# Kernel optimization log

Measured on AMD Instinct MI355X. Metric: run time of the kernel, lower is better.

The kernel has to match this reference:

```python
import jax, jax.numpy as jnp
import numpy as np

B, N, D = 8, 65536, 3
K = 64                 # num_centers
NPOINT = 4096
M = NPOINT // K * 2    # max_neighbors = 128
S = NPOINT // K        # fps samples per group = 64
NITER = 10             # KMeans default Niter


def _sqdist(src, dst):
    # ||s||^2 + ||d||^2 - 2 s.d   (same math as (s-d)^2 sum, GEMM form)
    s2 = (src ** 2).sum(-1)[:, :, None]          # [B,N,1]
    d2 = (dst ** 2).sum(-1)[:, None, :]          # [B,1,K]
    return s2 + d2 - 2.0 * jnp.einsum('bnd,bkd->bnk', src, dst)


def _kmeans(x):
    Bb, Nn, Dd = x.shape
    c = x[:, :K, :]
    bidx = jnp.arange(Bb)[:, None]               # broadcast with cl [B,N]
    for _ in range(NITER):
        cl = jnp.argmin(_sqdist(x, c), axis=2)   # [B,N] cluster codes
        c = jnp.zeros((Bb, K, Dd), x.dtype).at[bidx, cl].add(x)
        ncl = jnp.zeros((Bb, K), x.dtype).at[bidx, cl].add(1.0)
        c = c / ncl[:, :, None]
    return c


def _query_neighbor(x, centers):
    dist = _sqdist(x, centers)                   # [B,N,K]
    negd = -jnp.transpose(dist, (0, 2, 1))       # [B,K,N]
    _, nidx = jax.lax.top_k(negd, M)             # M nearest points per center
    bidx = jnp.arange(x.shape[0])[:, None, None]
    return x[bidx, nidx]                         # [B,K,M,3]


def _batch_fps(xyz, farthest0):
    # xyz: [B,G,Nn,3]; sequential farthest-point sampling per group
    Bb, G, Nn, _ = xyz.shape
    dist0 = jnp.full((Bb, G, Nn), 1e10, xyz.dtype)

    def step(carry, _):
        distance, farthest = carry
        centroid = jnp.take_along_axis(xyz, farthest[:, :, None, None], axis=2)  # [B,G,1,3]
        d = ((xyz - centroid) ** 2).sum(-1)       # [B,G,Nn]
        distance = jnp.minimum(distance, d)
        new_far = jnp.argmax(distance, -1).astype(farthest.dtype)
        return (distance, new_far), farthest      # store index BEFORE update

    _, idx = jax.lax.scan(step, (dist0, farthest0), None, length=S)
    idx = jnp.transpose(idx, (1, 2, 0))           # [B,G,S]
    idx3 = jnp.broadcast_to(idx[..., None], idx.shape + (3,))
    new_xyz = jnp.take_along_axis(xyz, idx3, axis=2)  # [B,G,S,3]
    return new_xyz.reshape(Bb, G * S, 3)


def setup_inputs() -> dict:
    key = jax.random.key(0)
    k1, k2 = jax.random.split(key)
    x = jax.random.normal(k1, (B, N, D), dtype=jnp.float32)
    farthest0 = jax.random.randint(k2, (B, K), 0, M, dtype=jnp.int32)
    return {"x": x, "farthest0": farthest0}


def reference(x, farthest0):
    centers = _kmeans(x)                  # [B,K,3]
    neighbor = _query_neighbor(x, centers)  # [B,K,M,3]
    new_xyz = _batch_fps(neighbor, farthest0)  # [B, NPOINT, 3]
    return new_xyz, centers
```

## Files before the change

kernel.cpp:

```cpp
#include <hip/hip_runtime.h>
#include <stdint.h>

#pragma clang fp contract(off)

#define B 8
#define N 65536
#define KC 64
#define M 128
#define S 64
#define NITER 10
#define HPAD 257
#define SAMPLE 8192
#define SCAP 2048
#define CAPG 3072
#define WCAP 512
#define CSTRIDE 32
#define NCHK 64
#define SUMB 2048

using u32 = unsigned int;
using u64 = unsigned long long;

__device__ __forceinline__ float sq3(float a, float b, float c) {
  return __fadd_rn(__fadd_rn(__fmul_rn(a, a), __fmul_rn(b, b)), __fmul_rn(c, c));
}
__device__ __forceinline__ float dot3(float x0, float x1, float x2,
                                      float c0, float c1, float c2) {
  return __fadd_rn(__fadd_rn(__fmul_rn(x0, c0), __fmul_rn(x1, c1)), __fmul_rn(x2, c2));
}
__device__ __forceinline__ float distf(float s2, float d2, float dt) {
  return __fsub_rn(__fadd_rn(s2, d2), __fmul_rn(2.0f, dt));
}
__device__ __forceinline__ u32 fkey(float f) {
  u32 u = __float_as_uint(f);
  return (u & 0x80000000u) ? ~u : (u | 0x80000000u);
}


__global__ void k_init_centers(const float* __restrict__ x, float* __restrict__ centers) {
  int i = blockIdx.x * blockDim.x + threadIdx.x;
  if (i >= B * KC * 3) return;
  int b = i / (KC * 3);
  int r = i % (KC * 3);
  centers[i] = x[(size_t)b * N * 3 + r];
}

__global__ __launch_bounds__(256)
void k_assign(const float* __restrict__ x, const float* __restrict__ centers,
              unsigned char* __restrict__ cl, u32* __restrict__ counts) {
  __shared__ float4 cs[KC];
  __shared__ int lh[KC];
  int g = blockIdx.x;
  int b = g & 7;
  int chunk = g >> 3;
  int t = threadIdx.x;
  if (t < KC) {
    float a0 = centers[(b * KC + t) * 3 + 0];
    float a1 = centers[(b * KC + t) * 3 + 1];
    float a2 = centers[(b * KC + t) * 3 + 2];
    cs[t] = make_float4(a0, a1, a2, sq3(a0, a1, a2));
    lh[t] = 0;
  }
  __syncthreads();
  int q = chunk * 256 + t;
  const float4* xb4 = (const float4*)(x + (size_t)b * N * 3);
  float4 A = xb4[3 * q], Bv = xb4[3 * q + 1], C = xb4[3 * q + 2];
  float p0x = A.x, p0y = A.y, p0z = A.z;
  float p1x = A.w, p1y = Bv.x, p1z = Bv.y;
  float p2x = Bv.z, p2y = Bv.w, p2z = C.x;
  float p3x = C.y, p3y = C.z, p3z = C.w;
  float s0 = sq3(p0x, p0y, p0z);
  float s1 = sq3(p1x, p1y, p1z);
  float s2 = sq3(p2x, p2y, p2z);
  float s3 = sq3(p3x, p3y, p3z);
  float inf = __int_as_float(0x7f800000);
  float b0 = inf, b1 = inf, b2 = inf, b3 = inf;
  int i0 = 0, i1 = 0, i2 = 0, i3 = 0;
  for (int k = 0; k < KC; ++k) {
    float4 cc = cs[k];
    float d0 = distf(s0, cc.w, dot3(p0x, p0y, p0z, cc.x, cc.y, cc.z));
    float d1 = distf(s1, cc.w, dot3(p1x, p1y, p1z, cc.x, cc.y, cc.z));
    float d2 = distf(s2, cc.w, dot3(p2x, p2y, p2z, cc.x, cc.y, cc.z));
    float d3 = distf(s3, cc.w, dot3(p3x, p3y, p3z, cc.x, cc.y, cc.z));
    if (d0 < b0) { b0 = d0; i0 = k; }
    if (d1 < b1) { b1 = d1; i1 = k; }
    if (d2 < b2) { b2 = d2; i2 = k; }
    if (d3 < b3) { b3 = d3; i3 = k; }
  }
  *(u32*)(cl + (size_t)b * N + 4 * q) =
      (u32)i0 | ((u32)i1 << 8) | ((u32)i2 << 16) | ((u32)i3 << 24);
  atomicAdd(&lh[i0], 1); atomicAdd(&lh[i1], 1);
  atomicAdd(&lh[i2], 1); atomicAdd(&lh[i3], 1);
  __syncthreads();
  if (t < KC) counts[(size_t)((b << 6) | chunk) * KC + t] = (u32)lh[t];
}

__global__ __launch_bounds__(256)
void k_scatter_stable(const float* __restrict__ x, const unsigned char* __restrict__ cl,
                      const u32* __restrict__ counts, float* __restrict__ sortedPts) {
  __shared__ int destBase[KC];
  __shared__ u32 wcnt[4][KC];
  int g = blockIdx.x;
  int b = g & 7, c = g >> 3;
  int t = threadIdx.x, lane = t & 63, wid = t >> 6;
  if (t < KC) {
    int bp = 0, tot = 0;
    for (int j = 0; j < NCHK; ++j) {
      int v = (int)counts[(size_t)((b << 6) | j) * KC + t];
      if (j < c) bp += v;
      tot += v;
    }
    int incl = tot;
#pragma unroll
    for (int o = 1; o < 64; o <<= 1) {
      int u = __shfl_up(incl, o);
      if (lane >= o) incl += u;
    }
    destBase[t] = (incl - tot) + bp;
  }
  int q = c * 256 + t;
  const float4* xb4 = (const float4*)(x + (size_t)b * N * 3);
  float4 A = xb4[3 * q], Bv = xb4[3 * q + 1], C2 = xb4[3 * q + 2];
  u32 word = *(const u32*)(cl + (size_t)b * N + 4 * (size_t)q);
  u32 kk0 = word & 255u, kk1 = (word >> 8) & 255u;
  u32 kk2 = (word >> 16) & 255u, kk3 = (word >> 24) & 255u;
  u64 ltm = ((u64)1 << lane) - 1;
  u32 rk0 = 0, rk1 = 0, rk2 = 0, rk3 = 0;
  for (int k = 0; k < KC; ++k) {
    u64 m0 = __ballot(kk0 == (u32)k), m1 = __ballot(kk1 == (u32)k);
    u64 m2 = __ballot(kk2 == (u32)k), m3 = __ballot(kk3 == (u32)k);
    u32 low = (u32)(__popcll(m0 & ltm) + __popcll(m1 & ltm) +
                    __popcll(m2 & ltm) + __popcll(m3 & ltm));
    u32 x0 = (u32)((m0 >> lane) & 1), x1 = (u32)((m1 >> lane) & 1);
    u32 x2 = (u32)((m2 >> lane) & 1);
    if (kk0 == (u32)k) rk0 = low;
    if (kk1 == (u32)k) rk1 = low + x0;
    if (kk2 == (u32)k) rk2 = low + x0 + x1;
    if (kk3 == (u32)k) rk3 = low + x0 + x1 + x2;
    if (lane == 0)
      wcnt[wid][k] = (u32)(__popcll(m0) + __popcll(m1) + __popcll(m2) + __popcll(m3));
  }
  __syncthreads();
  float px[4] = {A.x, A.w, Bv.z, C2.y};
  float py[4] = {A.y, Bv.x, Bv.w, C2.z};
  float pz[4] = {A.z, Bv.y, C2.x, C2.w};
  u32 kks[4] = {kk0, kk1, kk2, kk3};
  u32 rks[4] = {rk0, rk1, rk2, rk3};
#pragma unroll
  for (int s = 0; s < 4; ++s) {
    u32 k = kks[s];
    u32 r = rks[s];
#pragma unroll
    for (int w2 = 0; w2 < 3; ++w2) if (w2 < wid) r += wcnt[w2][k];
    int dest = destBase[k] + (int)r;
    float* dp = sortedPts + ((size_t)b * N + dest) * 3;
    dp[0] = px[s]; dp[1] = py[s]; dp[2] = pz[s];
  }
}

__global__ __launch_bounds__(256)
void k_sum_centers(const float* __restrict__ sortedPts, const u32* __restrict__ counts,
                   float* __restrict__ centers) {
  __shared__ float buf0[SUMB * 3], buf1[SUMB * 3];
  __shared__ int sLo, sCnt;
  int g = blockIdx.x;
  int bk = ((g & 7) << 6) | (g >> 3);
  int b = bk >> 6, k = bk & 63;
  int t = threadIdx.x, lane = t & 63;
  if (t < 64) {
    int tot = 0;
    for (int j = 0; j < NCHK; ++j)
      tot += (int)counts[(size_t)((b << 6) | j) * KC + t];
    int incl = tot;
#pragma unroll
    for (int o = 1; o < 64; o <<= 1) {
      int u = __shfl_up(incl, o);
      if (lane >= o) incl += u;
    }
    if (t == k) { sLo = incl - tot; sCnt = tot; }
  }
  __syncthreads();
  int lo = sLo, cnt = sCnt;
  const float* sp = sortedPts + ((size_t)b * N + lo) * 3;
  int nch = (cnt + SUMB - 1) / SUMB;
  if (t >= 64) {
    int nf = min(SUMB, cnt) * 3;
    for (int i = t - 64; i < nf; i += 192) buf0[i] = sp[i];
  }
  __syncthreads();
  float acc = 0.f;
  for (int z = 0; z < nch; ++z) {
    if (t >= 64) {
      if (z + 1 < nch) {
        float* d = ((z + 1) & 1) ? buf1 : buf0;
        int base = (z + 1) * SUMB;
        int nf = min(SUMB, cnt - base) * 3;
        const float* s2 = sp + (size_t)base * 3;
        for (int i = t - 64; i < nf; i += 192) d[i] = s2[i];
      }
    } else if (t < 3) {
      const float* bb = (z & 1) ? buf1 : buf0;
      int bn = min(SUMB, cnt - z * SUMB);
#pragma unroll 8
      for (int i = 0; i < bn; ++i)
        acc = __fadd_rn(acc, bb[3 * i + t]);
    }
    __syncthreads();
  }
  if (t < 3) centers[bk * 3 + t] = __fdiv_rn(acc, (float)cnt);
}

__global__ __launch_bounds__(256)
void k_thresh(const float* __restrict__ x, const float* __restrict__ centers,
              u32* __restrict__ thr, u32* __restrict__ cnt) {
  __shared__ u32 whist[4 * HPAD];
  __shared__ int sv[256];
  __shared__ u32 skeys[SCAP];
  __shared__ float4 scen;
  __shared__ u32 sSel;
  __shared__ int sNeed, sCntBin, sNum;
  int g = blockIdx.x;
  int bk = ((g & 7) << 6) | (g >> 3);
  int b = bk >> 6;
  int t = threadIdx.x, wid = t >> 6;
  if (t == 0) {
    float c0 = centers[bk * 3], c1 = centers[bk * 3 + 1], c2 = centers[bk * 3 + 2];
    scen = make_float4(c0, c1, c2, sq3(c0, c1, c2));
    cnt[bk * CSTRIDE] = 0;
    sNum = 0;
  }
  for (int i = t; i < 4 * HPAD; i += 256) whist[i] = 0;
  __syncthreads();
  float c0 = scen.x, c1 = scen.y, c2 = scen.z, d2 = scen.w;
  const float2* xb2 = (const float2*)(x + (size_t)b * N * 3);

  for (int p = t; p < SAMPLE / 2; p += 256) {
    float2 A = xb2[3 * p], Bv = xb2[3 * p + 1], C = xb2[3 * p + 2];
    float d0 = distf(sq3(A.x, A.y, Bv.x), d2, dot3(A.x, A.y, Bv.x, c0, c1, c2));
    float d1 = distf(sq3(Bv.y, C.x, C.y), d2, dot3(Bv.y, C.x, C.y, c0, c1, c2));
    atomicAdd(&whist[wid * HPAD + (fkey(d0) >> 24)], 1u);
    atomicAdd(&whist[wid * HPAD + (fkey(d1) >> 24)], 1u);
  }
  __syncthreads();
  int own = (int)(whist[0 * HPAD + t] + whist[1 * HPAD + t] +
                  whist[2 * HPAD + t] + whist[3 * HPAD + t]);
  sv[t] = own;
  __syncthreads();
  for (int off = 1; off < 256; off <<= 1) {
    int add = (t >= off) ? sv[t - off] : 0;
    __syncthreads();
    sv[t] += add;
    __syncthreads();
  }
  if (sv[t] >= M && sv[t] - own < M) {
    sSel = (u32)t; sNeed = M - (sv[t] - own); sCntBin = own;
  }
  __syncthreads();
  u32 selByte = sSel;
  int need = sNeed;
  int cntBin = sCntBin;
  u32 prefix = selByte << 24;

  if (cntBin <= SCAP) {
    for (int p = t; p < SAMPLE / 2; p += 256) {
      float2 A = xb2[3 * p], Bv = xb2[3 * p + 1], C = xb2[3 * p + 2];
      float d0 = distf(sq3(A.x, A.y, Bv.x), d2, dot3(A.x, A.y, Bv.x, c0, c1, c2));
      float d1 = distf(sq3(Bv.y, C.x, C.y), d2, dot3(Bv.y, C.x, C.y, c0, c1, c2));
      u32 k0 = fkey(d0), k1 = fkey(d1);
      if ((k0 >> 24) == selByte) skeys[atomicAdd(&sNum, 1)] = k0;
      if ((k1 >> 24) == selByte) skeys[atomicAdd(&sNum, 1)] = k1;
    }
    __syncthreads();
    int ne = sNum;
    for (int sh = 16; sh >= 0; sh -= 8) {
      whist[t] = 0;
      __syncthreads();
      for (int i = t; i < ne; i += 256) {
        u32 kkk = skeys[i];
        if ((kkk >> (sh + 8)) == (prefix >> (sh + 8)))
          atomicAdd(&whist[(kkk >> sh) & 255u], 1u);
      }
      __syncthreads();
      int own2 = (int)whist[t];
      sv[t] = own2;
      __syncthreads();
      for (int off = 1; off < 256; off <<= 1) {
        int add = (t >= off) ? sv[t - off] : 0;
        __syncthreads();
        sv[t] += add;
        __syncthreads();
      }
      if (sv[t] >= need && sv[t] - own2 < need) {
        sSel = prefix | ((u32)t << sh);
        sNeed = need - (sv[t] - own2);
      }
      __syncthreads();
      prefix = sSel; need = sNeed;
      __syncthreads();
    }
    if (t == 0) thr[bk] = prefix;
  } else {
    if (t == 0) thr[bk] = prefix | 0x00FFFFFFu;
  }
}

__global__ __launch_bounds__(256)
void k_scatter_test(const float* __restrict__ x, const float* __restrict__ centers,
                    const u32* __restrict__ thr, u32* __restrict__ cnt,
                    u32* __restrict__ cand) {
  __shared__ float4 cs[KC];
  __shared__ u32 lthr[KC];
  __shared__ u64 wm0[4][KC], wm1[4][KC];
  __shared__ u32 wbase[4][KC];
  int g = blockIdx.x;
  int b = g & 7;
  int chunk = g >> 3;
  int t = threadIdx.x, lane = t & 63, wid = t >> 6;
  if (t < KC) {
    float a0 = centers[(b * KC + t) * 3 + 0];
    float a1 = centers[(b * KC + t) * 3 + 1];
    float a2 = centers[(b * KC + t) * 3 + 2];
    cs[t] = make_float4(a0, a1, a2, sq3(a0, a1, a2));
    lthr[t] = thr[b * KC + t];
  }
  __syncthreads();
  int pr = chunk * 256 + t;
  const float2* xb2 = (const float2*)(x + (size_t)b * N * 3);
  float2 A = xb2[3 * pr], Bv = xb2[3 * pr + 1], C = xb2[3 * pr + 2];
  float s20 = sq3(A.x, A.y, Bv.x);
  float s21 = sq3(Bv.y, C.x, C.y);
  u32 n0 = 2 * pr, n1 = 2 * pr + 1;
  u64 ltm = ((u64)1 << lane) - 1;

  for (int k = 0; k < KC; ++k) {
    float4 cc = cs[k];
    float d0 = distf(s20, cc.w, dot3(A.x, A.y, Bv.x, cc.x, cc.y, cc.z));
    float d1 = distf(s21, cc.w, dot3(Bv.y, C.x, C.y, cc.x, cc.y, cc.z));
    u64 m0 = __ballot(fkey(d0) <= lthr[k]);
    u64 m1 = __ballot(fkey(d1) <= lthr[k]);
    if (lane == 0) { wm0[wid][k] = m0; wm1[wid][k] = m1; }
  }
  __syncthreads();
  if (t < KC) {
    u32 pc[4];
    u32 total = 0;
#pragma unroll
    for (int w = 0; w < 4; ++w) {
      pc[w] = (u32)(__popcll(wm0[w][t]) + __popcll(wm1[w][t]));
      total += pc[w];
    }
    u32 base = (total > 0) ? atomicAdd(&cnt[(b * KC + t) * CSTRIDE], total) : 0u;
#pragma unroll
    for (int w = 0; w < 4; ++w) { wbase[w][t] = base; base += pc[w]; }
  }
  __syncthreads();
  u64 mybit = (u64)1 << lane;
  for (int k = 0; k < KC; ++k) {
    u64 m0 = wm0[wid][k], m1 = wm1[wid][k];
    if ((m0 | m1) == 0) continue;
    u32 wb = wbase[wid][k];
    u32* cb = cand + (size_t)(b * KC + k) * CAPG;
    if (m0 & mybit) {
      u32 pos = wb + (u32)__popcll(m0 & ltm);
      if (pos < CAPG) cb[pos] = n0;
    }
    if (m1 & mybit) {
      u32 pos = wb + (u32)__popcll(m0) + (u32)__popcll(m1 & ltm);
      if (pos < CAPG) cb[pos] = n1;
    }
  }
}

__global__ __launch_bounds__(256)
void k_topk_sort(const float* __restrict__ x, const float* __restrict__ centers,
                 const u32* __restrict__ cnt, const u32* __restrict__ cand,
                 float* __restrict__ neighbor) {
  __shared__ u64 candList[CAPG];
  __shared__ u32 hist[256];
  __shared__ u64 wbuf[WCAP];
  __shared__ u64 lessList[M];
  __shared__ u32 eqList[256];
  __shared__ u32 sSel;
  __shared__ int sNeed;
  __shared__ int cntW, cntLess, cntEq;
  __shared__ float4 scen;
  int g = blockIdx.x;
  int bk = ((g & 7) << 6) | (g >> 3);
  int b = bk >> 6;
  int t = threadIdx.x, lane = t & 63, wid = t >> 6;
  if (t == 0) {
    float c0 = centers[bk * 3], c1 = centers[bk * 3 + 1], c2 = centers[bk * 3 + 2];
    scen = make_float4(c0, c1, c2, sq3(c0, c1, c2));
    cntW = 0;
  }
  __syncthreads();
  float c0 = scen.x, c1 = scen.y, c2 = scen.z, d2 = scen.w;
  const float* xb = x + (size_t)b * N * 3;
  int cc = (int)cnt[bk * CSTRIDE];

  if (cc <= CAPG) {
    const u32* cb = cand + (size_t)bk * CAPG;
    for (int i = t; i < cc; i += 256) {
      u32 n = cb[i];
      float x0 = xb[n * 3], x1 = xb[n * 3 + 1], x2 = xb[n * 3 + 2];
      float d = distf(sq3(x0, x1, x2), d2, dot3(x0, x1, x2, c0, c1, c2));
      candList[i] = ((u64)fkey(d) << 32) | n;
    }
    __syncthreads();
    u32 prefix = 0;
    int need = M;
    for (int r = 3; r >= 0; --r) {
      int sh = r * 8;
      hist[t] = 0;
      __syncthreads();
      for (int i = t; i < cc; i += 256) {
        u32 key = (u32)(candList[i] >> 32);
        bool ok = (r == 3) || ((key >> (sh + 8)) == (prefix >> (sh + 8)));
        if (ok) atomicAdd(&hist[(key >> sh) & 255u], 1u);
      }
      __syncthreads();
      if (wid == 0) {
        u32 h0 = hist[4 * lane + 0], h1 = hist[4 * lane + 1];
        u32 h2 = hist[4 * lane + 2], h3 = hist[4 * lane + 3];
        u32 lsum = h0 + h1 + h2 + h3;
        u32 incl = lsum;
#pragma unroll
        for (int o = 1; o < 64; o <<= 1) {
          u32 u = __shfl_up(incl, o);
          if (lane >= o) incl += u;
        }
        u32 excl = incl - lsum;
        if ((int)excl < need && need <= (int)incl) {
          u32 hh[4] = {h0, h1, h2, h3};
          u32 cum = excl; int bin = -1; u32 bc = 0;
#pragma unroll
          for (int j = 0; j < 4; ++j) {
            if (bin < 0 && (int)(cum + hh[j]) >= need) { bin = 4 * lane + j; bc = cum; }
            cum += hh[j];
          }
          sSel = prefix | ((u32)bin << sh);
          sNeed = need - (int)bc;
        }
      }
      __syncthreads();
      prefix = sSel; need = sNeed;
      __syncthreads();
    }
    u32 K128 = prefix;
    for (int i = t; i < cc; i += 256) {
      u64 e = candList[i];
      if ((u32)(e >> 32) <= K128) {
        int p = atomicAdd(&cntW, 1);
        if (p < WCAP) wbuf[p] = e;
      }
    }
    __syncthreads();
    int wcnt2 = cntW;
    if (wcnt2 <= WCAP) {
      for (int i = t; i < WCAP; i += 256) if (i >= wcnt2) wbuf[i] = ~0ull;
      __syncthreads();
      for (int ksz = 2; ksz <= WCAP; ksz <<= 1) {
        for (int j = ksz >> 1; j > 0; j >>= 1) {
          for (int idx = t; idx < WCAP; idx += 256) {
            int ixj = idx ^ j;
            if (ixj > idx) {
              u64 a = wbuf[idx], bb = wbuf[ixj];
              bool up = ((idx & ksz) == 0);
              if (up ? (a > bb) : (a < bb)) { wbuf[idx] = bb; wbuf[ixj] = a; }
            }
          }
          __syncthreads();
        }
      }
      if (t < M) {
        int idx = (int)(wbuf[t] & 0xFFFFFFFFu);
        size_t src = ((size_t)b * N + idx) * 3;
        size_t dst = ((size_t)bk * M + t) * 3;
        neighbor[dst]     = x[src];
        neighbor[dst + 1] = x[src + 1];
        neighbor[dst + 2] = x[src + 2];
      }
      return;
    }
  }

  if (t == 0) { cntLess = 0; cntEq = 0; }
  __syncthreads();
  u32 prefix = 0;
  int need = M;
  for (int r = 3; r >= 0; --r) {
    for (int i = t; i < 256; i += 256) hist[i] = 0;
    __syncthreads();
    int sh = r * 8;
    for (int n = t; n < N; n += 256) {
      float x0 = xb[n * 3], x1 = xb[n * 3 + 1], x2 = xb[n * 3 + 2];
      float d = distf(sq3(x0, x1, x2), d2, dot3(x0, x1, x2, c0, c1, c2));
      u32 key = fkey(d);
      bool ok = (r == 3) || ((key >> (sh + 8)) == (prefix >> (sh + 8)));
      if (ok) atomicAdd(&hist[(key >> sh) & 255u], 1u);
    }
    __syncthreads();
    if (t == 0) {
      int cum = 0;
      for (int bin = 0; bin < 256; ++bin) {
        int ccv = (int)hist[bin];
        if (cum + ccv >= need) { sSel = prefix | ((u32)bin << sh); sNeed = need - cum; break; }
        cum += ccv;
      }
    }
    __syncthreads();
    prefix = sSel; need = sNeed;
    __syncthreads();
  }
  u32 K128 = prefix;

  for (int n = t; n < N; n += 256) {
    float x0 = xb[n * 3], x1 = xb[n * 3 + 1], x2 = xb[n * 3 + 2];
    float d = distf(sq3(x0, x1, x2), d2, dot3(x0, x1, x2, c0, c1, c2));
    u32 key = fkey(d);
    if (key < K128) {
      int p = atomicAdd(&cntLess, 1);
      if (p < M) lessList[p] = ((u64)key << 32) | (u32)n;
    } else if (key == K128) {
      int p = atomicAdd(&cntEq, 1);
      if (p < 256) eqList[p] = (u32)n;
    }
  }
  __syncthreads();
  int nl = cntLess;
  int ne2 = cntEq;
  for (int i = t; i < M; i += 256) if (i >= nl) lessList[i] = ~0ull;
  for (int i = t; i < 256; i += 256) if (i >= ne2) eqList[i] = 0xFFFFFFFFu;
  __syncthreads();

  for (int ksz = 2; ksz <= M; ksz <<= 1) {
    for (int j = ksz >> 1; j > 0; j >>= 1) {
      for (int idx = t; idx < M; idx += 256) {
        int ixj = idx ^ j;
        if (ixj > idx) {
          u64 a = lessList[idx], bb = lessList[ixj];
          bool up = ((idx & ksz) == 0);
          if (up ? (a > bb) : (a < bb)) { lessList[idx] = bb; lessList[ixj] = a; }
        }
      }
      __syncthreads();
    }
  }
  for (int ksz = 2; ksz <= 256; ksz <<= 1) {
    for (int j = ksz >> 1; j > 0; j >>= 1) {
      for (int idx = t; idx < 256; idx += 256) {
        int ixj = idx ^ j;
        if (ixj > idx) {
          u32 a = eqList[idx], bb = eqList[ixj];
          bool up = ((idx & ksz) == 0);
          if (up ? (a > bb) : (a < bb)) { eqList[idx] = bb; eqList[ixj] = a; }
        }
      }
      __syncthreads();
    }
  }

  if (t < M) {
    int idx = (t < nl) ? (int)(lessList[t] & 0xFFFFFFFFu) : (int)eqList[t - nl];
    size_t src = ((size_t)b * N + idx) * 3;
    size_t dst = ((size_t)bk * M + t) * 3;
    neighbor[dst]     = x[src];
    neighbor[dst + 1] = x[src + 1];
    neighbor[dst + 2] = x[src + 2];
  }
}

__global__ __launch_bounds__(64)
void k_fps(const float* __restrict__ neighbor, const int* __restrict__ farthest0,
           const float* __restrict__ centers, float* __restrict__ out) {
  __shared__ float4 pts[M];
  int bg = blockIdx.x;
  int b = bg >> 6, g = bg & 63;
  int t = threadIdx.x;
  {
    int i = bg * 64 + t;
    if (i < B * KC * 3) out[B * 4096 * 3 + i] = centers[i];
  }
  const float* nb = neighbor + (size_t)bg * M * 3;
  float ax = nb[6 * t],     ay = nb[6 * t + 1], az = nb[6 * t + 2];
  float bx = nb[6 * t + 3], by = nb[6 * t + 4], bz = nb[6 * t + 5];
  pts[2 * t]     = make_float4(ax, ay, az, 0.f);
  pts[2 * t + 1] = make_float4(bx, by, bz, 0.f);
  int far = farthest0[bg];
  float dist0 = 1e10f, dist1 = 1e10f;
  __syncthreads();
  float* ob = out + ((size_t)b * 4096 + g * 64) * 3;
  for (int s = 0; s < S; ++s) {
    if ((far >> 1) == t) {
      if (far & 1) { ob[3 * s] = bx; ob[3 * s + 1] = by; ob[3 * s + 2] = bz; }
      else         { ob[3 * s] = ax; ob[3 * s + 1] = ay; ob[3 * s + 2] = az; }
    }
    float4 cc = pts[far];
    float d0 = sq3(__fsub_rn(ax, cc.x), __fsub_rn(ay, cc.y), __fsub_rn(az, cc.z));
    float d1 = sq3(__fsub_rn(bx, cc.x), __fsub_rn(by, cc.y), __fsub_rn(bz, cc.z));
    dist0 = fminf(dist0, d0);
    dist1 = fminf(dist1, d1);
    u64 k0 = ((u64)__float_as_uint(dist0) << 32) | (u32)(M - 1 - 2 * t);
    u64 k1 = ((u64)__float_as_uint(dist1) << 32) | (u32)(M - 2 - 2 * t);
    u64 key = (k0 > k1) ? k0 : k1;
#pragma unroll
    for (int off = 1; off < 64; off <<= 1) {
      u64 o = __shfl_xor(key, off);
      if (o > key) key = o;
    }
    far = M - 1 - (int)(key & 0xFFFFFFFFu);
  }
}

extern "C" void kernel_launch(void* const* d_in, const int* in_sizes, int n_in,
                              void* d_out, int out_size, void* d_ws, size_t ws_size,
                              hipStream_t stream) {
  const float* x = (const float*)d_in[0];
  const int* farthest0 = (const int*)d_in[1];
  float* out = (float*)d_out;

  char* w = (char*)d_ws;
  float* centers  = (float*)(w);
  unsigned char* cl = (unsigned char*)(w + 8192);
  u32* thr        = (u32*)(w + 8192 + 524288);
  u32* cnt        = (u32*)(w + 8192 + 524288 + 4096);
  u32* counts     = (u32*)(w + 8192 + 524288 + 4096 + 65536);
  float* neighbor = (float*)(w + 8192 + 524288 + 4096 + 65536 + 131072);
  char* shared    = w + 8192 + 524288 + 4096 + 65536 + 131072 + 786432;
  float* sortedPts = (float*)shared;
  u32* cand        = (u32*)shared;

  k_init_centers<<<6, 256, 0, stream>>>(x, centers);
  for (int it = 0; it < NITER; ++it) {
    k_assign<<<B * NCHK, 256, 0, stream>>>(x, centers, cl, counts);
    k_scatter_stable<<<B * NCHK, 256, 0, stream>>>(x, cl, counts, sortedPts);
    k_sum_centers<<<B * KC, 256, 0, stream>>>(sortedPts, counts, centers);
  }
  k_thresh<<<B * KC, 256, 0, stream>>>(x, centers, thr, cnt);
  k_scatter_test<<<B * NCHK * 2, 256, 0, stream>>>(x, centers, thr, cnt, cand);
  k_topk_sort<<<B * KC, 256, 0, stream>>>(x, centers, cnt, cand, neighbor);
  k_fps<<<B * KC, M / 2, 0, stream>>>(neighbor, farthest0, centers, out);
}
```

Before: 563.0 us.

## Scatter 16-bit point indices instead of sorted coordinates in k-means update

The stable scatter now writes a 16-bit point index per sorted slot instead of copying three floats. The center-sum kernel gathers coordinates from x through those indices into a structure-of-arrays shared buffer with padding, and the chunk size is halved. This cuts scatter write traffic and the sorted-points buffer, but the sum kernel now does indirect, uncoalesced gathers from x.

```diff
diff --git a/kernel.cpp b/kernel.cpp
--- a/kernel.cpp
+++ b/kernel.cpp
@@ -16,10 +16,11 @@
 #define WCAP 512
 #define CSTRIDE 32
 #define NCHK 64
-#define SUMB 2048
+#define SUMB 1024
 
 using u32 = unsigned int;
 using u64 = unsigned long long;
+using u16 = unsigned short;
 
 __device__ __forceinline__ float sq3(float a, float b, float c) {
   return __fadd_rn(__fadd_rn(__fmul_rn(a, a), __fmul_rn(b, b)), __fmul_rn(c, c));
@@ -96,8 +97,8 @@
 }
 
 __global__ __launch_bounds__(256)
-void k_scatter_stable(const float* __restrict__ x, const unsigned char* __restrict__ cl,
-                      const u32* __restrict__ counts, float* __restrict__ sortedPts) {
+void k_scatter_idx(const unsigned char* __restrict__ cl,
+                   const u32* __restrict__ counts, u16* __restrict__ midxG) {
   __shared__ int destBase[KC];
   __shared__ u32 wcnt[4][KC];
   int g = blockIdx.x;
@@ -119,8 +120,6 @@
     destBase[t] = (incl - tot) + bp;
   }
   int q = c * 256 + t;
-  const float4* xb4 = (const float4*)(x + (size_t)b * N * 3);
-  float4 A = xb4[3 * q], Bv = xb4[3 * q + 1], C2 = xb4[3 * q + 2];
   u32 word = *(const u32*)(cl + (size_t)b * N + 4 * (size_t)q);
   u32 kk0 = word & 255u, kk1 = (word >> 8) & 255u;
   u32 kk2 = (word >> 16) & 255u, kk3 = (word >> 24) & 255u;
@@ -141,27 +140,24 @@
       wcnt[wid][k] = (u32)(__popcll(m0) + __popcll(m1) + __popcll(m2) + __popcll(m3));
   }
   __syncthreads();
-  float px[4] = {A.x, A.w, Bv.z, C2.y};
-  float py[4] = {A.y, Bv.x, Bv.w, C2.z};
-  float pz[4] = {A.z, Bv.y, C2.x, C2.w};
   u32 kks[4] = {kk0, kk1, kk2, kk3};
   u32 rks[4] = {rk0, rk1, rk2, rk3};
+  u16* mb = midxG + (size_t)b * N;
+  u32 base = (u32)(4 * q);
 #pragma unroll
   for (int s = 0; s < 4; ++s) {
     u32 k = kks[s];
     u32 r = rks[s];
 #pragma unroll
     for (int w2 = 0; w2 < 3; ++w2) if (w2 < wid) r += wcnt[w2][k];
-    int dest = destBase[k] + (int)r;
-    float* dp = sortedPts + ((size_t)b * N + dest) * 3;
-    dp[0] = px[s]; dp[1] = py[s]; dp[2] = pz[s];
+    mb[destBase[k] + (int)r] = (u16)(base + s);
   }
 }
 
 __global__ __launch_bounds__(256)
-void k_sum_centers(const float* __restrict__ sortedPts, const u32* __restrict__ counts,
-                   float* __restrict__ centers) {
-  __shared__ float buf0[SUMB * 3], buf1[SUMB * 3];
+void k_sum_centers(const float* __restrict__ x, const u16* __restrict__ midxG,
+                   const u32* __restrict__ counts, float* __restrict__ centers) {
+  __shared__ float buf[2][3][SUMB + 1];
   __shared__ int sLo, sCnt;
   int g = blockIdx.x;
   int bk = ((g & 7) << 6) | (g >> 3);
@@ -181,29 +177,39 @@
   }
   __syncthreads();
   int lo = sLo, cnt = sCnt;
-  const float* sp = sortedPts + ((size_t)b * N + lo) * 3;
+  const u16* mp = midxG + (size_t)b * N + lo;
+  const float* xb = x + (size_t)b * N * 3;
   int nch = (cnt + SUMB - 1) / SUMB;
   if (t >= 64) {
-    int nf = min(SUMB, cnt) * 3;
-    for (int i = t - 64; i < nf; i += 192) buf0[i] = sp[i];
+    int bn = min(SUMB, cnt);
+    for (int i = t - 64; i < bn; i += 192) {
+      int li = (int)mp[i];
+      buf[0][0][i] = xb[3 * li];
+      buf[0][1][i] = xb[3 * li + 1];
+      buf[0][2][i] = xb[3 * li + 2];
+    }
   }
   __syncthreads();
   float acc = 0.f;
   for (int z = 0; z < nch; ++z) {
     if (t >= 64) {
       if (z + 1 < nch) {
-        float* d = ((z + 1) & 1) ? buf1 : buf0;
         int base = (z + 1) * SUMB;
-        int nf = min(SUMB, cnt - base) * 3;
-        const float* s2 = sp + (size_t)base * 3;
-        for (int i = t - 64; i < nf; i += 192) d[i] = s2[i];
+        int bn = min(SUMB, cnt - base);
+        int pb = (z + 1) & 1;
+        for (int i = t - 64; i < bn; i += 192) {
+          int li = (int)mp[base + i];
+          buf[pb][0][i] = xb[3 * li];
+          buf[pb][1][i] = xb[3 * li + 1];
+          buf[pb][2][i] = xb[3 * li + 2];
+        }
       }
     } else if (t < 3) {
-      const float* bb = (z & 1) ? buf1 : buf0;
+      const float* bb = &buf[z & 1][t][0];
       int bn = min(SUMB, cnt - z * SUMB);
 #pragma unroll 8
       for (int i = 0; i < bn; ++i)
-        acc = __fadd_rn(acc, bb[3 * i + t]);
+        acc = __fadd_rn(acc, bb[i]);
     }
     __syncthreads();
   }
@@ -627,14 +633,14 @@
   u32* counts     = (u32*)(w + 8192 + 524288 + 4096 + 65536);
   float* neighbor = (float*)(w + 8192 + 524288 + 4096 + 65536 + 131072);
   char* shared    = w + 8192 + 524288 + 4096 + 65536 + 131072 + 786432;
-  float* sortedPts = (float*)shared;
-  u32* cand        = (u32*)shared;
+  u16* midxG      = (u16*)shared;
+  u32* cand       = (u32*)shared;
 
   k_init_centers<<<6, 256, 0, stream>>>(x, centers);
   for (int it = 0; it < NITER; ++it) {
     k_assign<<<B * NCHK, 256, 0, stream>>>(x, centers, cl, counts);
-    k_scatter_stable<<<B * NCHK, 256, 0, stream>>>(x, cl, counts, sortedPts);
-    k_sum_centers<<<B * KC, 256, 0, stream>>>(sortedPts, counts, centers);
+    k_scatter_idx<<<B * NCHK, 256, 0, stream>>>(cl, counts, midxG);
+    k_sum_centers<<<B * KC, 256, 0, stream>>>(x, midxG, counts, centers);
   }
   k_thresh<<<B * KC, 256, 0, stream>>>(x, centers, thr, cnt);
   k_scatter_test<<<B * NCHK * 2, 256, 0, stream>>>(x, centers, thr, cnt, cand);
```

Result: no change. 552.4 us (-1.9%).
